# Kernel tuning notes

Hardware: AMD Instinct MI355X
Metric: run time of the kernel (lower is better)

Reference implementation:

```python
import jax, jax.numpy as jnp
import numpy as np

# Config: num_elems=64, num_attrs=8, vocab=1024, max_len=16, hidden=1024,
# input_embedding_dim=64, output_embedding_dim=256, num_layers=1, LSTM cell,
# attention=False, peeky=False, message=None, eval mode (argmax sampling).
B, A, NE = 2048, 8, 64
EIN, EOUT, H, V, L = 64, 256, 1024, 1024, 16


def setup_inputs() -> dict:
    key = jax.random.key(0)
    ks = jax.random.split(key, 12)
    s = 0.05
    return {
        "x": jax.random.randint(ks[0], (B, A), 0, NE),
        "in_emb": jax.random.normal(ks[1], (NE, EIN), jnp.float32) * s,
        "out_emb": jax.random.normal(ks[2], (V, EOUT), jnp.float32) * s,
        "W_in": jax.random.normal(ks[3], (H, A * EIN), jnp.float32) * s,
        "b_in": jnp.zeros((H,), jnp.float32),
        "W_ih": jax.random.normal(ks[4], (4 * H, EOUT), jnp.float32) * s,
        "b_ih": jnp.zeros((4 * H,), jnp.float32),
        "W_hh": jax.random.normal(ks[5], (4 * H, H), jnp.float32) * s,
        "b_hh": jnp.zeros((4 * H,), jnp.float32),
        "W_out": jax.random.normal(ks[6], (V, H), jnp.float32) * s,
        "b_out": jnp.zeros((V,), jnp.float32),
        "sos": jax.random.normal(ks[7], (EOUT,), jnp.float32),
    }


def reference(x, in_emb, out_emb, W_in, b_in, W_ih, b_ih, W_hh, b_hh, W_out, b_out, sos):
    bsz = x.shape[0]
    # input embedding -> concat attrs -> initial hidden
    ie = in_emb[x].reshape(bsz, -1)              # [B, A*EIN]
    h0 = ie @ W_in.T + b_in                      # [B, H]
    c0 = jnp.zeros_like(h0)                      # LSTM cell state starts at 0
    emb0 = jnp.broadcast_to(sos, (bsz, sos.shape[0]))  # SOS embedding [B, EOUT]

    def step(carry, _):
        h, c, emb = carry
        gates = emb @ W_ih.T + b_ih + h @ W_hh.T + b_hh  # [B, 4H], torch gate order i,f,g,o
        i, f, g, o = jnp.split(gates, 4, axis=-1)
        c_new = jax.nn.sigmoid(f) * c + jax.nn.sigmoid(i) * jnp.tanh(g)
        h_new = jax.nn.sigmoid(o) * jnp.tanh(c_new)
        logits = h_new @ W_out.T + b_out                 # [B, V]
        symbol = jnp.argmax(logits, axis=-1)             # eval-mode greedy sampling
        return (h_new, c_new, out_emb[symbol]), (symbol, logits)

    _, (syms, logits) = jax.lax.scan(step, (h0, c0, emb0), None, length=L)
    sequence = syms.T                                    # [B, L]
    logits = jnp.transpose(logits, (1, 0, 2))            # [B, L, V]
    return sequence, logits
```

## Files before the change

kernel.cpp:

```cpp
#include <hip/hip_runtime.h>
#include <math.h>

constexpr int kB    = 2048;
constexpr int kA    = 8;
constexpr int kEin  = 64;
constexpr int kEout = 256;
constexpr int kH    = 1024;
constexpr int kV    = 1024;
constexpr int kL    = 16;
constexpr int kKin  = kA * kEin;
constexpr int kKg   = kEout + kH;
constexpr int kNG   = 4 * kH;
constexpr float kInvLo = 1.0f / 2048.0f;

using half8 = __attribute__((ext_vector_type(8))) _Float16;
using half4 = __attribute__((ext_vector_type(4))) _Float16;
using f32x4 = __attribute__((ext_vector_type(4))) float;

#define GLL16(g, l) __builtin_amdgcn_global_load_lds(                        \
    (const __attribute__((address_space(1))) void*)(g),                      \
    (__attribute__((address_space(3))) void*)(l), 16, 0, 0)
#define SCHEDB() __builtin_amdgcn_sched_barrier(0)

__device__ __forceinline__ float sigm(float x) { return 1.0f / (1.0f + expf(-x)); }

struct HL { _Float16 hi, lo; };
__device__ __forceinline__ HL split2v(float x) {
  HL r;
  r.hi = (_Float16)x;
  r.lo = (_Float16)((x - (float)r.hi) * 2048.0f);
  return r;
}

__global__ __launch_bounds__(256) void init_state(float* __restrict__ c,
                                                  int* __restrict__ sym) {
  int i = blockIdx.x * 256 + threadIdx.x;
  c[i] = 0.0f;
  if (i < kB) sym[i] = kV;
}

__global__ __launch_bounds__(256) void split_plain(const float* __restrict__ src,
                                                   _Float16* __restrict__ hi,
                                                   _Float16* __restrict__ lo,
                                                   int n4) {
  int i = blockIdx.x * 256 + threadIdx.x;
  if (i >= n4) return;
  float4 v = ((const float4*)src)[i];
  half4 h, l;
  HL s0 = split2v(v.x), s1 = split2v(v.y), s2 = split2v(v.z), s3 = split2v(v.w);
  h.x = s0.hi; l.x = s0.lo; h.y = s1.hi; l.y = s1.lo;
  h.z = s2.hi; l.z = s2.lo; h.w = s3.hi; l.w = s3.lo;
  *(half4*)(hi + (size_t)i * 4) = h;
  *(half4*)(lo + (size_t)i * 4) = l;
}

__global__ __launch_bounds__(320) void split_gates_w(const float* __restrict__ W_ih,
                                                     const float* __restrict__ W_hh,
                                                     _Float16* __restrict__ hi,
                                                     _Float16* __restrict__ lo) {
  const int n  = blockIdx.x;
  const int k4 = threadIdx.x * 4;
  const int g  = (n >> 4) & 3;
  const int j  = ((n >> 6) << 4) | (n & 15);
  const int src = g * kH + j;
  float4 v = (k4 < kEout) ? *(const float4*)&W_ih[(size_t)src * kEout + k4]
                          : *(const float4*)&W_hh[(size_t)src * kH + (k4 - kEout)];
  half4 h, l;
  HL s0 = split2v(v.x), s1 = split2v(v.y), s2 = split2v(v.z), s3 = split2v(v.w);
  h.x = s0.hi; l.x = s0.lo; h.y = s1.hi; l.y = s1.lo;
  h.z = s2.hi; l.z = s2.lo; h.w = s3.hi; l.w = s3.lo;
  *(half4*)(hi + (size_t)n * kKg + k4) = h;
  *(half4*)(lo + (size_t)n * kKg + k4) = l;
}

__global__ __launch_bounds__(256) void h0_gemm(const int* __restrict__ x,
                                               const float* __restrict__ in_emb,
                                               const float* __restrict__ W_in,
                                               const float* __restrict__ b_in,
                                               _Float16* __restrict__ h_hi,
                                               _Float16* __restrict__ h_lo) {
  __shared__ float As[16][128];
  __shared__ float Bs[16][128];
  const int t  = threadIdx.x;
  const int tx = t & 15, ty = t >> 4;
  const int r  = t >> 1;
  const int kc = (t & 1) * 8;
  const int m0 = blockIdx.x * 128;
  const int n0 = blockIdx.y * 128;
  float acc[8][8] = {};
  for (int k0 = 0; k0 < kKin; k0 += 16) {
    const int kk   = k0 + kc;
    const int attr = kk >> 6;
    const int e    = kk & 63;
    const int idx  = x[(m0 + r) * kA + attr];
    const float* pa = in_emb + (size_t)idx * kEin + e;
    float4 a0 = *(const float4*)pa;
    float4 a1 = *(const float4*)(pa + 4);
    const float* pb = W_in + (size_t)(n0 + r) * kKin + kk;
    float4 b0 = *(const float4*)pb;
    float4 b1 = *(const float4*)(pb + 4);
    __syncthreads();
    As[kc+0][r]=a0.x; As[kc+1][r]=a0.y; As[kc+2][r]=a0.z; As[kc+3][r]=a0.w;
    As[kc+4][r]=a1.x; As[kc+5][r]=a1.y; As[kc+6][r]=a1.z; As[kc+7][r]=a1.w;
    Bs[kc+0][r]=b0.x; Bs[kc+1][r]=b0.y; Bs[kc+2][r]=b0.z; Bs[kc+3][r]=b0.w;
    Bs[kc+4][r]=b1.x; Bs[kc+5][r]=b1.y; Bs[kc+6][r]=b1.z; Bs[kc+7][r]=b1.w;
    __syncthreads();
#pragma unroll
    for (int k = 0; k < 16; ++k) {
      float a[8], b[8];
      *(float4*)&a[0] = *(const float4*)&As[k][ty*8];
      *(float4*)&a[4] = *(const float4*)&As[k][ty*8+4];
      *(float4*)&b[0] = *(const float4*)&Bs[k][tx*8];
      *(float4*)&b[4] = *(const float4*)&Bs[k][tx*8+4];
#pragma unroll
      for (int i = 0; i < 8; ++i)
#pragma unroll
        for (int j = 0; j < 8; ++j)
          acc[i][j] = fmaf(a[i], b[j], acc[i][j]);
    }
  }
#pragma unroll
  for (int i = 0; i < 8; ++i) {
    const int gm = m0 + ty*8 + i;
#pragma unroll
    for (int j = 0; j < 8; ++j) {
      const int gn = n0 + tx*8 + j;
      HL s = split2v(acc[i][j] + b_in[gn]);
      h_hi[(size_t)gm * kH + gn] = s.hi;
      h_lo[(size_t)gm * kH + gn] = s.lo;
    }
  }
}

__global__ __launch_bounds__(256, 2) void eg_gemm(
    const _Float16* __restrict__ oe_hi, const _Float16* __restrict__ oe_lo,
    const _Float16* __restrict__ Wg_hi, const _Float16* __restrict__ Wg_lo,
    float* __restrict__ Eg) {
  __shared__ __align__(16) _Float16 Ah[4][128][8], Al[4][128][8],
                                    Bh[4][128][8], Bl[4][128][8];
  const int t    = threadIdx.x;
  const int m0   = blockIdx.x * 128;
  const int by   = blockIdx.y;
  const int n0   = by * 128;
  const int r    = t & 127, q = t >> 7;
  const int rw   = r & 64;
  const int lane = t & 63, wid = t >> 6;
  const int wm   = (wid >> 1) * 64;
  const int wnv  = wid & 1;
  const int lc   = lane & 15, lg = lane >> 4;
  f32x4 acc1[4][4] = {}; f32x4 acc2[4][4] = {};
  for (int k0 = 0; k0 < kEout; k0 += 32) {
    const size_t oa = (size_t)(m0 + r) * kEout + k0 + q * 16;
    const size_t ob = (size_t)(n0 + r) * kKg + k0 + q * 16;
    __syncthreads();
    GLL16(oe_hi + oa,     &Ah[2*q  ][rw][0]);
    GLL16(oe_hi + oa + 8, &Ah[2*q+1][rw][0]);
    GLL16(oe_lo + oa,     &Al[2*q  ][rw][0]);
    GLL16(oe_lo + oa + 8, &Al[2*q+1][rw][0]);
    GLL16(Wg_hi + ob,     &Bh[2*q  ][rw][0]);
    GLL16(Wg_hi + ob + 8, &Bh[2*q+1][rw][0]);
    GLL16(Wg_lo + ob,     &Bl[2*q  ][rw][0]);
    GLL16(Wg_lo + ob + 8, &Bl[2*q+1][rw][0]);
    __syncthreads();
    half8 ah[4], al[4], bh[4], bl[4];
#pragma unroll
    for (int mf = 0; mf < 4; ++mf) {
      ah[mf] = *(const half8*)&Ah[lg][wm + mf*16 + lc][0];
      al[mf] = *(const half8*)&Al[lg][wm + mf*16 + lc][0];
    }
#pragma unroll
    for (int nf = 0; nf < 4; ++nf) {
      bh[nf] = *(const half8*)&Bh[lg][wnv*64 + nf*16 + lc][0];
      bl[nf] = *(const half8*)&Bl[lg][wnv*64 + nf*16 + lc][0];
    }
#pragma unroll
    for (int mf = 0; mf < 4; ++mf)
#pragma unroll
      for (int nf = 0; nf < 4; ++nf) {
        acc1[mf][nf] = __builtin_amdgcn_mfma_f32_16x16x32_f16(ah[mf], bh[nf], acc1[mf][nf], 0, 0, 0);
        acc2[mf][nf] = __builtin_amdgcn_mfma_f32_16x16x32_f16(ah[mf], bl[nf], acc2[mf][nf], 0, 0, 0);
        acc2[mf][nf] = __builtin_amdgcn_mfma_f32_16x16x32_f16(al[mf], bh[nf], acc2[mf][nf], 0, 0, 0);
      }
  }
#pragma unroll
  for (int mf = 0; mf < 4; ++mf)
#pragma unroll
    for (int reg = 0; reg < 4; ++reg) {
      const int m = m0 + wm + mf * 16 + lg * 4 + reg;
#pragma unroll
      for (int nf = 0; nf < 4; ++nf)
        Eg[(size_t)m * kNG + n0 + wnv*64 + nf*16 + lc] =
            acc1[mf][nf][reg] + acc2[mf][nf][reg] * kInvLo;
    }
}

__global__ __launch_bounds__(256) void gs_row(const float* __restrict__ sos,
                                              const float* __restrict__ W_ih,
                                              float* __restrict__ Eg) {
  const int n = blockIdx.x * 256 + threadIdx.x;
  const int g = (n >> 4) & 3;
  const int j = ((n >> 6) << 4) | (n & 15);
  const float* w = W_ih + (size_t)(g * kH + j) * kEout;
  float s = 0.0f;
#pragma unroll 4
  for (int k = 0; k < kEout; k += 4) {
    float4 wv = *(const float4*)&w[k];
    float4 sv = *(const float4*)&sos[k];
    s += wv.x*sv.x + wv.y*sv.y + wv.z*sv.z + wv.w*sv.w;
  }
  Eg[(size_t)kV * kNG + n] = s;
}

__global__ __launch_bounds__(256, 2) void gates_lstm_mfma(
    const _Float16* __restrict__ h_hi,   const _Float16* __restrict__ h_lo,
    const _Float16* __restrict__ Wg_hi,  const _Float16* __restrict__ Wg_lo,
    const float* __restrict__ Eg,        const int* __restrict__ sym,
    const float* __restrict__ b_ih, const float* __restrict__ b_hh,
    float* __restrict__ c,
    _Float16* __restrict__ ho_hi, _Float16* __restrict__ ho_lo) {
  __shared__ __align__(16) _Float16 Ah[4][128][8], Al[4][128][8],
                                    Bh[4][128][8], Bl[4][128][8];
  __shared__ int syms[128];
  const int t    = threadIdx.x;
  const int m0   = blockIdx.x * 128;
  const int by   = blockIdx.y;
  const int n0   = by * 128;
  const int r    = t & 127, q = t >> 7;
  const int rw   = r & 64;
  const int lane = t & 63,  wid = t >> 6;
  const int wm   = (wid >> 1) * 64;
  const int wnv  = wid & 1;
  const int lc   = lane & 15, lg = lane >> 4;

  if (t < 128) syms[t] = sym[m0 + t];

  f32x4 acc1[4][4] = {}; f32x4 acc2[4][4] = {};
  for (int k0 = 0; k0 < kH; k0 += 32) {
    const size_t oa = (size_t)(m0 + r) * kH + k0 + q * 16;
    const size_t ob = (size_t)(n0 + r) * kKg + kEout + k0 + q * 16;
    __syncthreads();
    GLL16(h_hi + oa,     &Ah[2*q  ][rw][0]);
    GLL16(h_hi + oa + 8, &Ah[2*q+1][rw][0]);
    GLL16(h_lo + oa,     &Al[2*q  ][rw][0]);
    GLL16(h_lo + oa + 8, &Al[2*q+1][rw][0]);
    GLL16(Wg_hi + ob,     &Bh[2*q  ][rw][0]);
    GLL16(Wg_hi + ob + 8, &Bh[2*q+1][rw][0]);
    GLL16(Wg_lo + ob,     &Bl[2*q  ][rw][0]);
    GLL16(Wg_lo + ob + 8, &Bl[2*q+1][rw][0]);
    __syncthreads();
    half8 ah[4], al[4], bh[4], bl[4];
#pragma unroll
    for (int mf = 0; mf < 4; ++mf) {
      ah[mf] = *(const half8*)&Ah[lg][wm + mf*16 + lc][0];
      al[mf] = *(const half8*)&Al[lg][wm + mf*16 + lc][0];
    }
#pragma unroll
    for (int nf = 0; nf < 4; ++nf) {
      bh[nf] = *(const half8*)&Bh[lg][wnv*64 + nf*16 + lc][0];
      bl[nf] = *(const half8*)&Bl[lg][wnv*64 + nf*16 + lc][0];
    }
#pragma unroll
    for (int mf = 0; mf < 4; ++mf)
#pragma unroll
      for (int nf = 0; nf < 4; ++nf) {
        acc1[mf][nf] = __builtin_amdgcn_mfma_f32_16x16x32_f16(ah[mf], bh[nf], acc1[mf][nf], 0, 0, 0);
        acc2[mf][nf] = __builtin_amdgcn_mfma_f32_16x16x32_f16(ah[mf], bl[nf], acc2[mf][nf], 0, 0, 0);
        acc2[mf][nf] = __builtin_amdgcn_mfma_f32_16x16x32_f16(al[mf], bh[nf], acc2[mf][nf], 0, 0, 0);
      }
  }
  const int j = by * 32 + wnv * 16 + lc;
  const int nbase = n0 + wnv * 64 + lc;
  float bb[4];
#pragma unroll
  for (int nf = 0; nf < 4; ++nf) bb[nf] = b_ih[nf * kH + j] + b_hh[nf * kH + j];
#pragma unroll
  for (int mf = 0; mf < 4; ++mf)
#pragma unroll
    for (int reg = 0; reg < 4; ++reg) {
      const int lr = wm + mf * 16 + lg * 4 + reg;
      const int m  = m0 + lr;
      const size_t off = (size_t)m * kH + j;
      const float* Erow = Eg + (size_t)syms[lr] * kNG + nbase;
      const float vi = acc1[mf][0][reg] + acc2[mf][0][reg] * kInvLo + bb[0] + Erow[0];
      const float vf = acc1[mf][1][reg] + acc2[mf][1][reg] * kInvLo + bb[1] + Erow[16];
      const float vg = acc1[mf][2][reg] + acc2[mf][2][reg] * kInvLo + bb[2] + Erow[32];
      const float vo = acc1[mf][3][reg] + acc2[mf][3][reg] * kInvLo + bb[3] + Erow[48];
      const float cn = sigm(vf) * c[off] + sigm(vi) * tanhf(vg);
      const float hn = sigm(vo) * tanhf(cn);
      c[off] = cn;
      HL s = split2v(hn);
      ho_hi[off] = s.hi; ho_lo[off] = s.lo;
    }
}

__global__ __launch_bounds__(256, 2) void logits_mfma(
    const _Float16* __restrict__ h_hi, const _Float16* __restrict__ h_lo,
    const _Float16* __restrict__ Wo_hi, const _Float16* __restrict__ Wo_lo,
    const float* __restrict__ b_out, float* __restrict__ out) {
  __shared__ __align__(16) _Float16 Ah[2][4][64][8], Al[2][4][64][8],
                                    Bh[2][4][64][8], Bl[2][4][64][8];
  const int t    = threadIdx.x;
  const int m0   = blockIdx.x * 64, n0 = blockIdx.y * 64;
  const int lane = t & 63, wid = t >> 6;
  const int lc   = lane & 15, lg = lane >> 4;
  const int wr   = wid >> 1, wc = wid & 1;
  const int isB  = wid >> 1;
  const int kq   = (wid & 1) * 2;

  auto stage = [&](int p, int k0) {
    if (isB == 0) {
      const size_t o = (size_t)(m0 + lane) * kH + k0 + kq * 8;
      GLL16(h_hi + o,      &Ah[p][kq  ][0][0]);
      GLL16(h_hi + o + 8,  &Ah[p][kq+1][0][0]);
      GLL16(h_lo + o,      &Al[p][kq  ][0][0]);
      GLL16(h_lo + o + 8,  &Al[p][kq+1][0][0]);
    } else {
      const size_t o = (size_t)(n0 + lane) * kH + k0 + kq * 8;
      GLL16(Wo_hi + o,     &Bh[p][kq  ][0][0]);
      GLL16(Wo_hi + o + 8, &Bh[p][kq+1][0][0]);
      GLL16(Wo_lo + o,     &Bl[p][kq  ][0][0]);
      GLL16(Wo_lo + o + 8, &Bl[p][kq+1][0][0]);
    }
  };

  f32x4 acc1[2][2] = {}; f32x4 acc2[2][2] = {};
  constexpr int NK = kH / 32;
  stage(0, 0);
  for (int ks = 0; ks < NK; ++ks) {
    const int cur = ks & 1;
    if (ks + 1 < NK) {
      stage(cur ^ 1, (ks + 1) * 32);
      SCHEDB();
      asm volatile("s_waitcnt vmcnt(4)");
    } else {
      SCHEDB();
      asm volatile("s_waitcnt vmcnt(0)");
    }
    SCHEDB();
    __builtin_amdgcn_s_barrier();
    SCHEDB();
    half8 ah[2], al[2], bh[2], bl[2];
#pragma unroll
    for (int mf = 0; mf < 2; ++mf) {
      ah[mf] = *(const half8*)&Ah[cur][lg][wr*32 + mf*16 + lc][0];
      al[mf] = *(const half8*)&Al[cur][lg][wr*32 + mf*16 + lc][0];
    }
#pragma unroll
    for (int nf = 0; nf < 2; ++nf) {
      bh[nf] = *(const half8*)&Bh[cur][lg][wc*32 + nf*16 + lc][0];
      bl[nf] = *(const half8*)&Bl[cur][lg][wc*32 + nf*16 + lc][0];
    }
#pragma unroll
    for (int mf = 0; mf < 2; ++mf)
#pragma unroll
      for (int nf = 0; nf < 2; ++nf) {
        acc1[mf][nf] = __builtin_amdgcn_mfma_f32_16x16x32_f16(ah[mf], bh[nf], acc1[mf][nf], 0, 0, 0);
        acc2[mf][nf] = __builtin_amdgcn_mfma_f32_16x16x32_f16(ah[mf], bl[nf], acc2[mf][nf], 0, 0, 0);
        acc2[mf][nf] = __builtin_amdgcn_mfma_f32_16x16x32_f16(al[mf], bh[nf], acc2[mf][nf], 0, 0, 0);
      }
    SCHEDB();
    __builtin_amdgcn_s_barrier();
  }
#pragma unroll
  for (int mf = 0; mf < 2; ++mf)
#pragma unroll
    for (int reg = 0; reg < 4; ++reg) {
      const int m = m0 + wr*32 + mf * 16 + lg * 4 + reg;
#pragma unroll
      for (int nf = 0; nf < 2; ++nf) {
        const int n = n0 + wc*32 + nf * 16 + lc;
        out[(size_t)m * (kL * kV) + n] = acc1[mf][nf][reg] + acc2[mf][nf][reg] * kInvLo + b_out[n];
      }
    }
}

__global__ __launch_bounds__(256) void argmax_gather(const float* __restrict__ logits_t,
                                                     float* __restrict__ seq,
                                                     int* __restrict__ sym,
                                                     int t) {
  const int lane = threadIdx.x & 63;
  const int wv   = threadIdx.x >> 6;
  const int b    = blockIdx.x * 4 + wv;
  const float* row = logits_t + (size_t)b * (kL * kV);
  float m = -3.4e38f;
  int  mi = 0;
#pragma unroll
  for (int jr = 0; jr < kV / 64; ++jr) {
    const int idx = jr * 64 + lane;
    const float v = row[idx];
    if (v > m) { m = v; mi = idx; }
  }
#pragma unroll
  for (int off = 32; off > 0; off >>= 1) {
    const float om = __shfl_down(m, off);
    const int   oi = __shfl_down(mi, off);
    if (om > m || (om == m && oi < mi)) { m = om; mi = oi; }
  }
  if (lane == 0) {
    seq[(size_t)b * kL + t] = (float)mi;
    sym[b] = mi;
  }
}

extern "C" void kernel_launch(void* const* d_in, const int* in_sizes, int n_in,
                              void* d_out, int out_size, void* d_ws, size_t ws_size,
                              hipStream_t stream) {
  const int*   x       = (const int*)d_in[0];
  const float* in_emb  = (const float*)d_in[1];
  const float* out_emb = (const float*)d_in[2];
  const float* W_in    = (const float*)d_in[3];
  const float* b_in    = (const float*)d_in[4];
  const float* W_ih    = (const float*)d_in[5];
  const float* b_ih    = (const float*)d_in[6];
  const float* W_hh    = (const float*)d_in[7];
  const float* b_hh    = (const float*)d_in[8];
  const float* W_out   = (const float*)d_in[9];
  const float* b_out   = (const float*)d_in[10];
  const float* sos     = (const float*)d_in[11];

  float* cb  = (float*)d_ws;
  float* Eg  = cb + (size_t)kB * kH;
  int*   sym = (int*)(Eg + (size_t)(kV + 1) * kNG);
  _Float16* hp = (_Float16*)(sym + kB);
  const size_t nBH = (size_t)kB * kH;
  _Float16* hA_hi  = hp;            _Float16* hA_lo  = hp + nBH;
  _Float16* hB_hi  = hp + 2*nBH;    _Float16* hB_lo  = hp + 3*nBH;
  _Float16* Wg_hi  = hp + 4*nBH;
  _Float16* Wg_lo  = Wg_hi + (size_t)kNG*kKg;
  _Float16* Wo_hi  = Wg_lo + (size_t)kNG*kKg;
  _Float16* Wo_lo  = Wo_hi + (size_t)kV*kH;
  _Float16* oe_hi  = Wo_lo + (size_t)kV*kH;
  _Float16* oe_lo  = oe_hi + (size_t)kV*kEout;

  float* seq    = (float*)d_out;
  float* logits = seq + (size_t)kB * kL;

  init_state<<<(kB * kH) / 256, 256, 0, stream>>>(cb, sym);
  split_gates_w<<<kNG, 320, 0, stream>>>(W_ih, W_hh, Wg_hi, Wg_lo);
  split_plain<<<(kV * kH / 4) / 256, 256, 0, stream>>>(W_out, Wo_hi, Wo_lo, kV * kH / 4);
  split_plain<<<(kV * kEout / 4) / 256, 256, 0, stream>>>(out_emb, oe_hi, oe_lo, kV * kEout / 4);
  eg_gemm<<<dim3(kV / 128, kNG / 128), 256, 0, stream>>>(oe_hi, oe_lo, Wg_hi, Wg_lo, Eg);
  gs_row<<<kNG / 256, 256, 0, stream>>>(sos, W_ih, Eg);
  h0_gemm<<<dim3(kB / 128, kH / 128), 256, 0, stream>>>(x, in_emb, W_in, b_in, hA_hi, hA_lo);

  for (int t = 0; t < kL; ++t) {
    const _Float16* hi_h = (t & 1) ? hB_hi : hA_hi;
    const _Float16* hi_l = (t & 1) ? hB_lo : hA_lo;
    _Float16* ho_h = (t & 1) ? hA_hi : hB_hi;
    _Float16* ho_l = (t & 1) ? hA_lo : hB_lo;
    gates_lstm_mfma<<<dim3(kB / 128, kNG / 128), 256, 0, stream>>>(
        hi_h, hi_l, Wg_hi, Wg_lo, Eg, sym, b_ih, b_hh, cb, ho_h, ho_l);
    logits_mfma<<<dim3(kB / 64, kV / 64), 256, 0, stream>>>(
        ho_h, ho_l, Wo_hi, Wo_lo, b_out, logits + (size_t)t * kV);
    argmax_gather<<<kB / 4, 256, 0, stream>>>(logits + (size_t)t * kV, seq, sym, t);
  }
}
```

Before: 2.008 ms.

## Pre-pack h and weights into MFMA fragment layout and load directly from global

Hidden state and the W_hh/W_out weights are stored in a tiled fragment-major layout, so each wave's MFMA operands are contiguous 16-byte chunks. The gates and logits GEMMs then read operands straight from global memory into registers, dropping LDS staging, barriers and the double-buffer pipeline. The logits grid is also retiled from 64x64 to 128x32 tiles. This removes LDS traffic and sync overhead, but loses the cross-wave operand sharing through LDS, so it leans on L1/L2 for reuse and has no explicit prefetch.

```diff
diff --git a/kernel.cpp b/kernel.cpp
--- a/kernel.cpp
+++ b/kernel.cpp
@@ -9,7 +9,6 @@
 constexpr int kV    = 1024;
 constexpr int kL    = 16;
 constexpr int kKin  = kA * kEin;
-constexpr int kKg   = kEout + kH;
 constexpr int kNG   = 4 * kH;
 constexpr float kInvLo = 1.0f / 2048.0f;
 
@@ -20,7 +19,6 @@
 #define GLL16(g, l) __builtin_amdgcn_global_load_lds(                        \
     (const __attribute__((address_space(1))) void*)(g),                      \
     (__attribute__((address_space(3))) void*)(l), 16, 0, 0)
-#define SCHEDB() __builtin_amdgcn_sched_barrier(0)
 
 __device__ __forceinline__ float sigm(float x) { return 1.0f / (1.0f + expf(-x)); }
 
@@ -30,6 +28,10 @@
   r.hi = (_Float16)x;
   r.lo = (_Float16)((x - (float)r.hi) * 2048.0f);
   return r;
+}
+
+__device__ __forceinline__ size_t packA(int m, int k) {
+  return ((((size_t)(m >> 7) * 32 + (k >> 5)) * 4 + ((k >> 3) & 3)) * 128 + (m & 127)) * 8 + (k & 7);
 }
 
 __global__ __launch_bounds__(256) void init_state(float* __restrict__ c,
@@ -56,8 +58,10 @@
 
 __global__ __launch_bounds__(320) void split_gates_w(const float* __restrict__ W_ih,
                                                      const float* __restrict__ W_hh,
-                                                     _Float16* __restrict__ hi,
-                                                     _Float16* __restrict__ lo) {
+                                                     _Float16* __restrict__ rm_hi,
+                                                     _Float16* __restrict__ rm_lo,
+                                                     _Float16* __restrict__ p_hi,
+                                                     _Float16* __restrict__ p_lo) {
   const int n  = blockIdx.x;
   const int k4 = threadIdx.x * 4;
   const int g  = (n >> 4) & 3;
@@ -69,8 +73,31 @@
   HL s0 = split2v(v.x), s1 = split2v(v.y), s2 = split2v(v.z), s3 = split2v(v.w);
   h.x = s0.hi; l.x = s0.lo; h.y = s1.hi; l.y = s1.lo;
   h.z = s2.hi; l.z = s2.lo; h.w = s3.hi; l.w = s3.lo;
-  *(half4*)(hi + (size_t)n * kKg + k4) = h;
-  *(half4*)(lo + (size_t)n * kKg + k4) = l;
+  if (k4 < kEout) {
+    *(half4*)(rm_hi + (size_t)n * kEout + k4) = h;
+    *(half4*)(rm_lo + (size_t)n * kEout + k4) = l;
+  } else {
+    const int kp = k4 - kEout;
+    const size_t ad = packA(n, kp);
+    *(half4*)(p_hi + ad) = h;
+    *(half4*)(p_lo + ad) = l;
+  }
+}
+
+__global__ __launch_bounds__(256) void split_pack_wo(const float* __restrict__ W_out,
+                                                     _Float16* __restrict__ hi,
+                                                     _Float16* __restrict__ lo) {
+  const int n  = blockIdx.x;
+  const int k4 = threadIdx.x * 4;
+  float4 v = *(const float4*)&W_out[(size_t)n * kH + k4];
+  half4 h, l;
+  HL s0 = split2v(v.x), s1 = split2v(v.y), s2 = split2v(v.z), s3 = split2v(v.w);
+  h.x = s0.hi; l.x = s0.lo; h.y = s1.hi; l.y = s1.lo;
+  h.z = s2.hi; l.z = s2.lo; h.w = s3.hi; l.w = s3.lo;
+  const size_t ad = ((((size_t)(n >> 5) * 32 + (k4 >> 5)) * 4 + ((k4 >> 3) & 3)) * 32
+                     + (n & 31)) * 8 + (k4 & 7);
+  *(half4*)(hi + ad) = h;
+  *(half4*)(lo + ad) = l;
 }
 
 __global__ __launch_bounds__(256) void h0_gemm(const int* __restrict__ x,
@@ -121,14 +148,17 @@
   }
 #pragma unroll
   for (int i = 0; i < 8; ++i) {
-    const int gm = m0 + ty*8 + i;
+    const int gm  = m0 + ty*8 + i;
+    const int gn0 = n0 + tx*8;
+    half8 h8, l8;
 #pragma unroll
     for (int j = 0; j < 8; ++j) {
-      const int gn = n0 + tx*8 + j;
-      HL s = split2v(acc[i][j] + b_in[gn]);
-      h_hi[(size_t)gm * kH + gn] = s.hi;
-      h_lo[(size_t)gm * kH + gn] = s.lo;
-    }
+      HL s = split2v(acc[i][j] + b_in[gn0 + j]);
+      h8[j] = s.hi; l8[j] = s.lo;
+    }
+    const size_t ad = packA(gm, gn0);
+    *(half8*)(h_hi + ad) = h8;
+    *(half8*)(h_lo + ad) = l8;
   }
 }
 
@@ -151,7 +181,7 @@
   f32x4 acc1[4][4] = {}; f32x4 acc2[4][4] = {};
   for (int k0 = 0; k0 < kEout; k0 += 32) {
     const size_t oa = (size_t)(m0 + r) * kEout + k0 + q * 16;
-    const size_t ob = (size_t)(n0 + r) * kKg + k0 + q * 16;
+    const size_t ob = (size_t)(n0 + r) * kEout + k0 + q * 16;
     __syncthreads();
     GLL16(oe_hi + oa,     &Ah[2*q  ][rw][0]);
     GLL16(oe_hi + oa + 8, &Ah[2*q+1][rw][0]);
@@ -212,52 +242,37 @@
 }
 
 __global__ __launch_bounds__(256, 2) void gates_lstm_mfma(
-    const _Float16* __restrict__ h_hi,   const _Float16* __restrict__ h_lo,
-    const _Float16* __restrict__ Wg_hi,  const _Float16* __restrict__ Wg_lo,
+    const _Float16* __restrict__ hp_hi,  const _Float16* __restrict__ hp_lo,
+    const _Float16* __restrict__ Wgp_hi, const _Float16* __restrict__ Wgp_lo,
     const float* __restrict__ Eg,        const int* __restrict__ sym,
     const float* __restrict__ b_ih, const float* __restrict__ b_hh,
     float* __restrict__ c,
     _Float16* __restrict__ ho_hi, _Float16* __restrict__ ho_lo) {
-  __shared__ __align__(16) _Float16 Ah[4][128][8], Al[4][128][8],
-                                    Bh[4][128][8], Bl[4][128][8];
-  __shared__ int syms[128];
   const int t    = threadIdx.x;
-  const int m0   = blockIdx.x * 128;
+  const int bx   = blockIdx.x;
   const int by   = blockIdx.y;
-  const int n0   = by * 128;
-  const int r    = t & 127, q = t >> 7;
-  const int rw   = r & 64;
-  const int lane = t & 63,  wid = t >> 6;
+  const int m0   = bx * 128;
+  const int lane = t & 63, wid = t >> 6;
   const int wm   = (wid >> 1) * 64;
   const int wnv  = wid & 1;
   const int lc   = lane & 15, lg = lane >> 4;
-
-  if (t < 128) syms[t] = sym[m0 + t];
+  constexpr int SK = 4 * 128 * 8;
+
+  size_t adr_a = (size_t)bx * 32 * SK + ((size_t)lg * 128 + wm + lc) * 8;
+  size_t adr_b = (size_t)by * 32 * SK + ((size_t)lg * 128 + wnv * 64 + lc) * 8;
 
   f32x4 acc1[4][4] = {}; f32x4 acc2[4][4] = {};
-  for (int k0 = 0; k0 < kH; k0 += 32) {
-    const size_t oa = (size_t)(m0 + r) * kH + k0 + q * 16;
-    const size_t ob = (size_t)(n0 + r) * kKg + kEout + k0 + q * 16;
-    __syncthreads();
-    GLL16(h_hi + oa,     &Ah[2*q  ][rw][0]);
-    GLL16(h_hi + oa + 8, &Ah[2*q+1][rw][0]);
-    GLL16(h_lo + oa,     &Al[2*q  ][rw][0]);
-    GLL16(h_lo + oa + 8, &Al[2*q+1][rw][0]);
-    GLL16(Wg_hi + ob,     &Bh[2*q  ][rw][0]);
-    GLL16(Wg_hi + ob + 8, &Bh[2*q+1][rw][0]);
-    GLL16(Wg_lo + ob,     &Bl[2*q  ][rw][0]);
-    GLL16(Wg_lo + ob + 8, &Bl[2*q+1][rw][0]);
-    __syncthreads();
+  for (int ks = 0; ks < 32; ++ks) {
     half8 ah[4], al[4], bh[4], bl[4];
 #pragma unroll
     for (int mf = 0; mf < 4; ++mf) {
-      ah[mf] = *(const half8*)&Ah[lg][wm + mf*16 + lc][0];
-      al[mf] = *(const half8*)&Al[lg][wm + mf*16 + lc][0];
+      ah[mf] = *(const half8*)(hp_hi + adr_a + mf * 128);
+      al[mf] = *(const half8*)(hp_lo + adr_a + mf * 128);
     }
 #pragma unroll
     for (int nf = 0; nf < 4; ++nf) {
-      bh[nf] = *(const half8*)&Bh[lg][wnv*64 + nf*16 + lc][0];
-      bl[nf] = *(const half8*)&Bl[lg][wnv*64 + nf*16 + lc][0];
+      bh[nf] = *(const half8*)(Wgp_hi + adr_b + nf * 128);
+      bl[nf] = *(const half8*)(Wgp_lo + adr_b + nf * 128);
     }
 #pragma unroll
     for (int mf = 0; mf < 4; ++mf)
@@ -267,9 +282,11 @@
         acc2[mf][nf] = __builtin_amdgcn_mfma_f32_16x16x32_f16(ah[mf], bl[nf], acc2[mf][nf], 0, 0, 0);
         acc2[mf][nf] = __builtin_amdgcn_mfma_f32_16x16x32_f16(al[mf], bh[nf], acc2[mf][nf], 0, 0, 0);
       }
-  }
-  const int j = by * 32 + wnv * 16 + lc;
-  const int nbase = n0 + wnv * 64 + lc;
+    adr_a += SK; adr_b += SK;
+  }
+  const int j   = by * 32 + wnv * 16 + lc;
+  const int nbase = by * 128 + wnv * 64 + lc;
+  const int jks = j >> 5, jq = (j >> 3) & 3, je = j & 7;
   float bb[4];
 #pragma unroll
   for (int nf = 0; nf < 4; ++nf) bb[nf] = b_ih[nf * kH + j] + b_hh[nf * kH + j];
@@ -280,7 +297,7 @@
       const int lr = wm + mf * 16 + lg * 4 + reg;
       const int m  = m0 + lr;
       const size_t off = (size_t)m * kH + j;
-      const float* Erow = Eg + (size_t)syms[lr] * kNG + nbase;
+      const float* Erow = Eg + (size_t)sym[m] * kNG + nbase;
       const float vi = acc1[mf][0][reg] + acc2[mf][0][reg] * kInvLo + bb[0] + Erow[0];
       const float vf = acc1[mf][1][reg] + acc2[mf][1][reg] * kInvLo + bb[1] + Erow[16];
       const float vg = acc1[mf][2][reg] + acc2[mf][2][reg] * kInvLo + bb[2] + Erow[32];
@@ -289,66 +306,40 @@
       const float hn = sigm(vo) * tanhf(cn);
       c[off] = cn;
       HL s = split2v(hn);
-      ho_hi[off] = s.hi; ho_lo[off] = s.lo;
+      const size_t ad = ((((size_t)bx * 32 + jks) * 4 + jq) * 128 + lr) * 8 + je;
+      ho_hi[ad] = s.hi; ho_lo[ad] = s.lo;
     }
 }
 
 __global__ __launch_bounds__(256, 2) void logits_mfma(
-    const _Float16* __restrict__ h_hi, const _Float16* __restrict__ h_lo,
-    const _Float16* __restrict__ Wo_hi, const _Float16* __restrict__ Wo_lo,
+    const _Float16* __restrict__ hp_hi, const _Float16* __restrict__ hp_lo,
+    const _Float16* __restrict__ Wop_hi, const _Float16* __restrict__ Wop_lo,
     const float* __restrict__ b_out, float* __restrict__ out) {
-  __shared__ __align__(16) _Float16 Ah[2][4][64][8], Al[2][4][64][8],
-                                    Bh[2][4][64][8], Bl[2][4][64][8];
   const int t    = threadIdx.x;
-  const int m0   = blockIdx.x * 64, n0 = blockIdx.y * 64;
+  const int bx   = blockIdx.x;
+  const int by   = blockIdx.y;
   const int lane = t & 63, wid = t >> 6;
+  const int wm   = wid * 32;
   const int lc   = lane & 15, lg = lane >> 4;
-  const int wr   = wid >> 1, wc = wid & 1;
-  const int isB  = wid >> 1;
-  const int kq   = (wid & 1) * 2;
-
-  auto stage = [&](int p, int k0) {
-    if (isB == 0) {
-      const size_t o = (size_t)(m0 + lane) * kH + k0 + kq * 8;
-      GLL16(h_hi + o,      &Ah[p][kq  ][0][0]);
-      GLL16(h_hi + o + 8,  &Ah[p][kq+1][0][0]);
-      GLL16(h_lo + o,      &Al[p][kq  ][0][0]);
-      GLL16(h_lo + o + 8,  &Al[p][kq+1][0][0]);
-    } else {
-      const size_t o = (size_t)(n0 + lane) * kH + k0 + kq * 8;
-      GLL16(Wo_hi + o,     &Bh[p][kq  ][0][0]);
-      GLL16(Wo_hi + o + 8, &Bh[p][kq+1][0][0]);
-      GLL16(Wo_lo + o,     &Bl[p][kq  ][0][0]);
-      GLL16(Wo_lo + o + 8, &Bl[p][kq+1][0][0]);
-    }
-  };
+  constexpr int SKA = 4 * 128 * 8;
+  constexpr int SKB = 4 * 32 * 8;
+
+  size_t adr_a = (size_t)bx * 32 * SKA + ((size_t)lg * 128 + wm + lc) * 8;
+  size_t adr_b = (size_t)by * 32 * SKB + ((size_t)lg * 32 + lc) * 8;
 
   f32x4 acc1[2][2] = {}; f32x4 acc2[2][2] = {};
-  constexpr int NK = kH / 32;
-  stage(0, 0);
-  for (int ks = 0; ks < NK; ++ks) {
-    const int cur = ks & 1;
-    if (ks + 1 < NK) {
-      stage(cur ^ 1, (ks + 1) * 32);
-      SCHEDB();
-      asm volatile("s_waitcnt vmcnt(4)");
-    } else {
-      SCHEDB();
-      asm volatile("s_waitcnt vmcnt(0)");
-    }
-    SCHEDB();
-    __builtin_amdgcn_s_barrier();
-    SCHEDB();
+#pragma unroll 2
+  for (int ks = 0; ks < 32; ++ks) {
     half8 ah[2], al[2], bh[2], bl[2];
 #pragma unroll
     for (int mf = 0; mf < 2; ++mf) {
-      ah[mf] = *(const half8*)&Ah[cur][lg][wr*32 + mf*16 + lc][0];
-      al[mf] = *(const half8*)&Al[cur][lg][wr*32 + mf*16 + lc][0];
+      ah[mf] = *(const half8*)(hp_hi + adr_a + mf * 128);
+      al[mf] = *(const half8*)(hp_lo + adr_a + mf * 128);
     }
 #pragma unroll
     for (int nf = 0; nf < 2; ++nf) {
-      bh[nf] = *(const half8*)&Bh[cur][lg][wc*32 + nf*16 + lc][0];
-      bl[nf] = *(const half8*)&Bl[cur][lg][wc*32 + nf*16 + lc][0];
+      bh[nf] = *(const half8*)(Wop_hi + adr_b + nf * 128);
+      bl[nf] = *(const half8*)(Wop_lo + adr_b + nf * 128);
     }
 #pragma unroll
     for (int mf = 0; mf < 2; ++mf)
@@ -358,17 +349,16 @@
         acc2[mf][nf] = __builtin_amdgcn_mfma_f32_16x16x32_f16(ah[mf], bl[nf], acc2[mf][nf], 0, 0, 0);
         acc2[mf][nf] = __builtin_amdgcn_mfma_f32_16x16x32_f16(al[mf], bh[nf], acc2[mf][nf], 0, 0, 0);
       }
-    SCHEDB();
-    __builtin_amdgcn_s_barrier();
+    adr_a += SKA; adr_b += SKB;
   }
 #pragma unroll
   for (int mf = 0; mf < 2; ++mf)
 #pragma unroll
     for (int reg = 0; reg < 4; ++reg) {
-      const int m = m0 + wr*32 + mf * 16 + lg * 4 + reg;
+      const int m = bx * 128 + wm + mf * 16 + lg * 4 + reg;
 #pragma unroll
       for (int nf = 0; nf < 2; ++nf) {
-        const int n = n0 + wc*32 + nf * 16 + lc;
+        const int n = by * 32 + nf * 16 + lc;
         out[(size_t)m * (kL * kV) + n] = acc1[mf][nf][reg] + acc2[mf][nf][reg] * kInvLo + b_out[n];
       }
     }
@@ -425,21 +415,23 @@
   const size_t nBH = (size_t)kB * kH;
   _Float16* hA_hi  = hp;            _Float16* hA_lo  = hp + nBH;
   _Float16* hB_hi  = hp + 2*nBH;    _Float16* hB_lo  = hp + 3*nBH;
-  _Float16* Wg_hi  = hp + 4*nBH;
-  _Float16* Wg_lo  = Wg_hi + (size_t)kNG*kKg;
-  _Float16* Wo_hi  = Wg_lo + (size_t)kNG*kKg;
-  _Float16* Wo_lo  = Wo_hi + (size_t)kV*kH;
-  _Float16* oe_hi  = Wo_lo + (size_t)kV*kH;
-  _Float16* oe_lo  = oe_hi + (size_t)kV*kEout;
+  _Float16* Wgrm_hi = hp + 4*nBH;
+  _Float16* Wgrm_lo = Wgrm_hi + (size_t)kNG*kEout;
+  _Float16* Wgp_hi  = Wgrm_lo + (size_t)kNG*kEout;
+  _Float16* Wgp_lo  = Wgp_hi + (size_t)kNG*kH;
+  _Float16* Wop_hi  = Wgp_lo + (size_t)kNG*kH;
+  _Float16* Wop_lo  = Wop_hi + (size_t)kV*kH;
+  _Float16* oe_hi   = Wop_lo + (size_t)kV*kH;
+  _Float16* oe_lo   = oe_hi + (size_t)kV*kEout;
 
   float* seq    = (float*)d_out;
   float* logits = seq + (size_t)kB * kL;
 
   init_state<<<(kB * kH) / 256, 256, 0, stream>>>(cb, sym);
-  split_gates_w<<<kNG, 320, 0, stream>>>(W_ih, W_hh, Wg_hi, Wg_lo);
-  split_plain<<<(kV * kH / 4) / 256, 256, 0, stream>>>(W_out, Wo_hi, Wo_lo, kV * kH / 4);
+  split_gates_w<<<kNG, 320, 0, stream>>>(W_ih, W_hh, Wgrm_hi, Wgrm_lo, Wgp_hi, Wgp_lo);
+  split_pack_wo<<<kV, 256, 0, stream>>>(W_out, Wop_hi, Wop_lo);
   split_plain<<<(kV * kEout / 4) / 256, 256, 0, stream>>>(out_emb, oe_hi, oe_lo, kV * kEout / 4);
-  eg_gemm<<<dim3(kV / 128, kNG / 128), 256, 0, stream>>>(oe_hi, oe_lo, Wg_hi, Wg_lo, Eg);
+  eg_gemm<<<dim3(kV / 128, kNG / 128), 256, 0, stream>>>(oe_hi, oe_lo, Wgrm_hi, Wgrm_lo, Eg);
   gs_row<<<kNG / 256, 256, 0, stream>>>(sos, W_ih, Eg);
   h0_gemm<<<dim3(kB / 128, kH / 128), 256, 0, stream>>>(x, in_emb, W_in, b_in, hA_hi, hA_lo);
 
@@ -449,9 +441,9 @@
     _Float16* ho_h = (t & 1) ? hA_hi : hB_hi;
     _Float16* ho_l = (t & 1) ? hA_lo : hB_lo;
     gates_lstm_mfma<<<dim3(kB / 128, kNG / 128), 256, 0, stream>>>(
-        hi_h, hi_l, Wg_hi, Wg_lo, Eg, sym, b_ih, b_hh, cb, ho_h, ho_l);
-    logits_mfma<<<dim3(kB / 64, kV / 64), 256, 0, stream>>>(
-        ho_h, ho_l, Wo_hi, Wo_lo, b_out, logits + (size_t)t * kV);
+        hi_h, hi_l, Wgp_hi, Wgp_lo, Eg, sym, b_ih, b_hh, cb, ho_h, ho_l);
+    logits_mfma<<<dim3(kB / 128, kV / 32), 256, 0, stream>>>(
+        ho_h, ho_l, Wop_hi, Wop_lo, b_out, logits + (size_t)t * kV);
     argmax_gather<<<kB / 4, 256, 0, stream>>>(logits + (size_t)t * kV, seq, sym, t);
   }
 }
```

New measurement: 1.813 ms. -9.7%, faster.
